# Optimization experiments

Hardware: AMD Instinct MI355X
Metric: run time of the kernel (lower is better)

The kernel has to match this reference:

```python
import jax, jax.numpy as jnp
import numpy as np

N = 50000      # nodes
E = 600000     # edges
DIN = 128      # dim_in
DOUT = 128     # dim_out (mulhead=1)
DG = 64        # dim_gate


def setup_inputs() -> dict:
    key = jax.random.key(0)
    ks = jax.random.split(key, 10)
    rows = jax.random.randint(ks[0], (E,), 0, N, dtype=jnp.int32)   # dest nodes
    cols = jax.random.randint(ks[1], (E,), 0, N, dtype=jnp.int32)   # src nodes
    vals = jax.random.uniform(ks[2], (E,), dtype=jnp.float32)       # adj_norm values
    feat = jax.random.normal(ks[3], (N, DIN), dtype=jnp.float32)
    s = 1.0 / np.sqrt(DIN)
    W0 = jax.random.normal(ks[4], (DIN, DOUT), dtype=jnp.float32) * s
    b0 = jnp.zeros((DOUT,), dtype=jnp.float32)
    W1 = jax.random.normal(ks[5], (DIN, DOUT), dtype=jnp.float32) * s
    b1 = jnp.zeros((DOUT,), dtype=jnp.float32)
    att = jax.random.normal(ks[6], (2 * DOUT,), dtype=jnp.float32) * 0.1  # attention param [1, 2*DOUT] flattened
    W_pool = jax.random.normal(ks[7], (DIN, DG), dtype=jnp.float32) * s    # weight_pool_gate
    W_gate = jax.random.normal(ks[8], (2 * DIN + DG, 1), dtype=jnp.float32) * 0.05  # weight_gate, mulhead=1
    offset0 = jnp.zeros((DOUT,), dtype=jnp.float32)
    scale0 = jnp.ones((DOUT,), dtype=jnp.float32)
    offset1 = jnp.zeros((DOUT,), dtype=jnp.float32)
    scale1 = jnp.ones((DOUT,), dtype=jnp.float32)
    return dict(rows=rows, cols=cols, vals=vals, feat=feat, W0=W0, b0=b0,
                W1=W1, b1=b1, att=att, W_pool=W_pool, W_gate=W_gate,
                offset0=offset0, scale0=scale0, offset1=offset1, scale1=scale1)


def _batch_norm(x, scale, offset):
    # per-node norm over the feature dim (unbiased=False), matching _batch_norm
    m = x.mean(axis=1, keepdims=True)
    v = x.var(axis=1, keepdims=True) + 1e-9
    return (x - m) * scale * jax.lax.rsqrt(v) + offset


def reference(rows, cols, vals, feat, W0, b0, W1, b1, att, W_pool, W_gate,
              offset0, scale0, offset1, scale1):
    n = feat.shape[0]
    d = W0.shape[1]
    # --- gate value (GaAN eq. 3) ---
    zj = feat @ W_pool                                   # [N, DG]
    neigh_zj = jax.ops.segment_max(zj[cols], rows, num_segments=n)  # per-row max over neighbors
    neigh_zj = jnp.where(jnp.isfinite(neigh_zj), neigh_zj, 0.0)     # empty rows -> zeros
    neigh_mean = jax.ops.segment_sum(vals[:, None] * feat[cols], rows, num_segments=n)  # spmm(adj, feat)
    gate = jnp.concatenate([feat, neigh_zj, neigh_mean], axis=1) @ W_gate  # [N, 1]
    # --- per-order feature transforms (order=1, mulhead=1) ---
    h0 = jax.nn.relu(feat @ W0 + b0)                     # order 0 (self)
    h1 = jax.nn.relu(feat @ W1 + b1)                     # order 1 (neighbor)
    # --- sparse attention aggregation ---
    a_self = jax.nn.leaky_relu(h0 @ att[:d], 0.2)        # [N]
    a_neigh = jax.nn.leaky_relu(h1 @ att[d:], 0.2)       # [N]
    e = a_self[rows] + a_neigh[cols]                     # per-edge score (replaces adj values)
    agg = jax.ops.segment_sum(e[:, None] * h1[cols], rows, num_segments=n)  # spmm(att_adj, h1)
    agg = agg * gate[:, :1]                              # gated
    # --- per-node batch norm, then 'mean' aggregation (sum of orders) ---
    return _batch_norm(h0, scale0, offset0) + _batch_norm(agg, scale1, offset1)
```

## Files before the change

kernel.cpp:

```cpp
#include <hip/hip_runtime.h>

#define DIN 128
#define DG 64

typedef __attribute__((ext_vector_type(8))) short short8;
typedef __attribute__((ext_vector_type(4))) float f32x4;

static __device__ __forceinline__ unsigned short f2bf(float x) {
    unsigned u = __builtin_bit_cast(unsigned, x);
    u = (u + 0x7FFF + ((u >> 16) & 1)) >> 16;
    return (unsigned short)u;
}
static __device__ __forceinline__ float bf2f(unsigned short s) {
    return __builtin_bit_cast(float, (unsigned)s << 16);
}

__global__ void k_deg(const int* __restrict__ rows, int* __restrict__ deg,
                      int* __restrict__ slot, int E) {
    int e = blockIdx.x * blockDim.x + threadIdx.x;
    if (e < E) slot[e] = atomicAdd(&deg[rows[e]], 1);
}

__global__ __launch_bounds__(1024) void k_scan1(const int* __restrict__ deg,
                                                int* __restrict__ rowptr,
                                                int* __restrict__ bsum, int n) {
    __shared__ int wsum[16];
    __shared__ int woff[16];
    int tid = threadIdx.x;
    int lane = tid & 63, w = tid >> 6;
    int i = blockIdx.x * 1024 + tid;
    int v = (i < n) ? deg[i] : 0;
    int x = v;
    #pragma unroll
    for (int off = 1; off < 64; off <<= 1) {
        int y = __shfl_up(x, off, 64);
        if (lane >= off) x += y;
    }
    if (lane == 63) wsum[w] = x;
    __syncthreads();
    if (w == 0) {
        int t = (lane < 16) ? wsum[lane] : 0;
        int xx = t;
        #pragma unroll
        for (int off = 1; off < 16; off <<= 1) {
            int y = __shfl_up(xx, off, 64);
            if (lane >= off) xx += y;
        }
        if (lane < 16) woff[lane] = xx - t;
    }
    __syncthreads();
    if (i < n) rowptr[i] = x - v + woff[w];
    if (tid == 1023) bsum[blockIdx.x] = woff[15] + wsum[15];
}

__global__ void k_scan2(const int* __restrict__ bsum, int* __restrict__ boff,
                        int* __restrict__ rowptr, int nb, int n) {
    int lane = threadIdx.x;
    int v = (lane < nb) ? bsum[lane] : 0;
    int x = v;
    #pragma unroll
    for (int off = 1; off < 64; off <<= 1) {
        int y = __shfl_up(x, off, 64);
        if (lane >= off) x += y;
    }
    boff[lane] = x - v;
    if (lane == 63) rowptr[n] = x;
}

__global__ void k_scan3(int* __restrict__ rowptr, const int* __restrict__ boff, int n) {
    int i = blockIdx.x * blockDim.x + threadIdx.x;
    if (i < n) rowptr[i] += boff[i >> 10];
}

__global__ __launch_bounds__(256) void k_wt(
    const float* __restrict__ W0, const float* __restrict__ W1,
    unsigned short* __restrict__ Bt) {
    int k = blockIdx.x;
    int c = threadIdx.x;
    const float* W = (c < 128) ? W0 : W1;
    Bt[c * 128 + k] = f2bf(W[k * 128 + (c & 127)]);
}

#define AS_LD 132
#define ALD 136
#define SMEM_BYTES 25088

static __device__ __forceinline__ void zj_body(
    const float* __restrict__ feat, const float* __restrict__ Wp,
    const float* __restrict__ Wg,
    float* __restrict__ zj, float* __restrict__ gpart, float* __restrict__ fdotg,
    int N, char* smem) {
    float* As = (float*)smem;
    float* Bs = (float*)(smem + 32 * AS_LD * 4);
    int tid = threadIdx.x;
    int tx = tid & 15, ty = tid >> 4;
    int m0 = blockIdx.x * 128;
    if (m0 >= N) return;
    float acc[8][4];
    #pragma unroll
    for (int r = 0; r < 8; ++r)
        #pragma unroll
        for (int c = 0; c < 4; ++c) acc[r][c] = 0.f;
    float gdot[8], fdot[8];
    #pragma unroll
    for (int r = 0; r < 8; ++r) { gdot[r] = 0.f; fdot[r] = 0.f; }
    for (int kc = 0; kc < 128; kc += 32) {
        for (int i = tid; i < 1024; i += 256) {
            int m = i >> 3, kq = (i & 7) << 2;
            int node = m0 + m;
            float4 f;
            if (node < N) f = *(const float4*)&feat[(size_t)node * 128 + kc + kq];
            else          f = make_float4(0.f, 0.f, 0.f, 0.f);
            As[(kq + 0) * AS_LD + m] = f.x;
            As[(kq + 1) * AS_LD + m] = f.y;
            As[(kq + 2) * AS_LD + m] = f.z;
            As[(kq + 3) * AS_LD + m] = f.w;
        }
        for (int i = tid; i < 512; i += 256) {
            int k = i >> 4, cq = (i & 15) << 2;
            *(float4*)&Bs[k * 64 + cq] = *(const float4*)&Wp[(size_t)(kc + k) * 64 + cq];
        }
        __syncthreads();
        #pragma unroll 8
        for (int kk = 0; kk < 32; ++kk) {
            const float* ar = &As[kk * AS_LD];
            float4 a0 = *(const float4*)(ar + 4 * tx);
            float4 a1 = *(const float4*)(ar + 64 + 4 * tx);
            float4 b0v = *(const float4*)&Bs[kk * 64 + 4 * ty];
            float a[8] = {a0.x, a0.y, a0.z, a0.w, a1.x, a1.y, a1.z, a1.w};
            #pragma unroll
            for (int r = 0; r < 8; ++r) {
                acc[r][0] += a[r] * b0v.x; acc[r][1] += a[r] * b0v.y;
                acc[r][2] += a[r] * b0v.z; acc[r][3] += a[r] * b0v.w;
            }
            float g1 = Wg[kc + kk];
            float g2 = Wg[192 + kc + kk];
            #pragma unroll
            for (int r = 0; r < 8; ++r) { gdot[r] += a[r] * g1; fdot[r] += a[r] * g2; }
        }
        __syncthreads();
    }
    #pragma unroll
    for (int r = 0; r < 8; ++r) {
        int node = m0 + ((r < 4) ? (4 * tx + r) : (64 + 4 * tx + (r - 4)));
        if (node >= N) continue;
        *(float4*)&zj[(size_t)node * 64 + 4 * ty] =
            make_float4(acc[r][0], acc[r][1], acc[r][2], acc[r][3]);
        if (ty == 0) { gpart[node] = gdot[r]; fdotg[node] = fdot[r]; }
    }
}

static __device__ __forceinline__ void mfma_body(
    const float* __restrict__ feat, const unsigned short* __restrict__ Bt,
    const float* __restrict__ b0, const float* __restrict__ b1,
    const float* __restrict__ att,
    float* __restrict__ h0, unsigned short* __restrict__ hb,
    float* __restrict__ a_self, float* __restrict__ a_neigh, int N, char* smem) {
    unsigned short* As = (unsigned short*)smem;
    float* sredA = (float*)(smem + 64 * ALD * 2);
    float* nredA = sredA + 128;
    int tid = threadIdx.x;
    int m0 = blockIdx.x * 64;
    for (int i = tid; i < 2048; i += 256) {
        int row = i >> 5, ch = i & 31;
        int node = m0 + row;
        float4 f;
        if (node < N) f = *(const float4*)&feat[(size_t)node * 128 + ch * 4];
        else          f = make_float4(0.f, 0.f, 0.f, 0.f);
        unsigned p0 = (unsigned)f2bf(f.x) | ((unsigned)f2bf(f.y) << 16);
        unsigned p1 = (unsigned)f2bf(f.z) | ((unsigned)f2bf(f.w) << 16);
        *(uint2*)&As[row * ALD + ch * 4] = make_uint2(p0, p1);
    }
    __syncthreads();
    int w = tid >> 6, lane = tid & 63;
    int lm = lane & 15, q = lane >> 4;
    f32x4 acc[4][4];
    #pragma unroll
    for (int rt = 0; rt < 4; ++rt)
        #pragma unroll
        for (int ct = 0; ct < 4; ++ct)
            #pragma unroll
            for (int r = 0; r < 4; ++r) acc[rt][ct][r] = 0.f;
    #pragma unroll
    for (int ks = 0; ks < 4; ++ks) {
        short8 a[4], b[4];
        #pragma unroll
        for (int rt = 0; rt < 4; ++rt)
            a[rt] = *(const short8*)&As[(rt * 16 + lm) * ALD + ks * 32 + q * 8];
        #pragma unroll
        for (int ct = 0; ct < 4; ++ct)
            b[ct] = *(const short8*)&Bt[(size_t)(w * 64 + ct * 16 + lm) * 128 + ks * 32 + q * 8];
        #pragma unroll
        for (int rt = 0; rt < 4; ++rt)
            #pragma unroll
            for (int ct = 0; ct < 4; ++ct)
                acc[rt][ct] = __builtin_amdgcn_mfma_f32_16x16x32_bf16(a[rt], b[ct], acc[rt][ct], 0, 0, 0);
    }
    float sacc[4][4];
    #pragma unroll
    for (int rt = 0; rt < 4; ++rt)
        #pragma unroll
        for (int r = 0; r < 4; ++r) sacc[rt][r] = 0.f;
    #pragma unroll
    for (int ct = 0; ct < 4; ++ct) {
        int col = w * 64 + ct * 16 + lm;
        float attc = att[col];
        float bias = (w < 2) ? b0[col] : b1[col - 128];
        #pragma unroll
        for (int rt = 0; rt < 4; ++rt) {
            #pragma unroll
            for (int r = 0; r < 4; ++r) {
                float v = acc[rt][ct][r] + bias;
                v = fmaxf(v, 0.f);
                sacc[rt][r] += v * attc;
                int node = m0 + rt * 16 + q * 4 + r;
                if (node < N) {
                    if (w < 2) h0[(size_t)node * 128 + col] = v;
                    else       hb[(size_t)node * 128 + (col - 128)] = f2bf(v);
                }
            }
        }
    }
    float* red = (w < 2) ? sredA : nredA;
    #pragma unroll
    for (int rt = 0; rt < 4; ++rt)
        #pragma unroll
        for (int r = 0; r < 4; ++r) {
            float s = sacc[rt][r];
            s += __shfl_xor(s, 1, 64); s += __shfl_xor(s, 2, 64);
            s += __shfl_xor(s, 4, 64); s += __shfl_xor(s, 8, 64);
            if (lm == 0) red[(w & 1) * 64 + rt * 16 + q * 4 + r] = s;
        }
    __syncthreads();
    if (tid < 64) {
        int node = m0 + tid;
        if (node < N) {
            float s  = sredA[tid] + sredA[64 + tid];
            float nn = nredA[tid] + nredA[64 + tid];
            a_self[node]  = (s  >= 0.f) ? s  : 0.2f * s;
            a_neigh[node] = (nn >= 0.f) ? nn : 0.2f * nn;
        }
    }
}

__global__ __launch_bounds__(256) void k_gemm_fused(
    const float* __restrict__ feat, const float* __restrict__ Wp,
    const unsigned short* __restrict__ Bt,
    const float* __restrict__ b0, const float* __restrict__ b1,
    const float* __restrict__ att, const float* __restrict__ Wg,
    float* __restrict__ h0, unsigned short* __restrict__ hb,
    float* __restrict__ zj, float* __restrict__ gpart, float* __restrict__ fdotg,
    float* __restrict__ a_self, float* __restrict__ a_neigh, int N) {
    __shared__ __align__(16) char smem[SMEM_BYTES];
    if (blockIdx.y == 0)
        zj_body(feat, Wp, Wg, zj, gpart, fdotg, N, smem);
    else
        mfma_body(feat, Bt, b0, b1, att, h0, hb, a_self, a_neigh, N, smem);
}

__global__ void k_scatter_meta(const int* __restrict__ rows, const int* __restrict__ cols,
                               const float* __restrict__ vals,
                               const int* __restrict__ rowptr, const int* __restrict__ slot,
                               const float* __restrict__ a_neigh, const float* __restrict__ fdotg,
                               float4* __restrict__ meta, int E) {
    int e = blockIdx.x * blockDim.x + threadIdx.x;
    if (e < E) {
        int c = cols[e];
        int dst = rowptr[rows[e]] + slot[e];
        meta[dst] = make_float4(__builtin_bit_cast(float, c),
                                a_neigh[c], vals[e] * fdotg[c], 0.f);
    }
}

template<int C>
static __device__ __forceinline__ void agg_chunk_m(
    const float4* __restrict__ meta, int j, int je, int lane, float asr,
    const unsigned short* __restrict__ hb, const float* __restrict__ zj,
    float2& acca, float& zmax, float& vfsum) {
    float4 m[C]; bool act[C];
    #pragma unroll
    for (int t = 0; t < C; ++t) {
        int jj = j + t;
        act[t] = jj < je;
        m[t] = meta[act[t] ? jj : (je - 1)];
    }
    ushort2 hv[C]; float zv[C];
    #pragma unroll
    for (int t = 0; t < C; ++t) {
        int c = __builtin_bit_cast(int, m[t].x);
        hv[t] = ((const ushort2*)(hb + (size_t)c * 128))[lane];
        zv[t] = zj[(size_t)c * 64 + lane];
    }
    #pragma unroll
    for (int t = 0; t < C; ++t) {
        float es = act[t] ? (asr + m[t].y) : 0.f;
        acca.x += es * bf2f(hv[t].x);
        acca.y += es * bf2f(hv[t].y);
        zmax = fmaxf(zmax, act[t] ? zv[t] : -__builtin_inff());
        vfsum += act[t] ? m[t].z : 0.f;
    }
}

__global__ __launch_bounds__(256) void k_aggregate(
    const float4* __restrict__ meta, const int* __restrict__ rowptr,
    const float* __restrict__ h0, const unsigned short* __restrict__ hb,
    const float* __restrict__ zj,
    const float* __restrict__ a_self, const float* __restrict__ gpart,
    const float* __restrict__ Wg,
    const float* __restrict__ scale0, const float* __restrict__ offset0,
    const float* __restrict__ scale1, const float* __restrict__ offset1,
    float* __restrict__ out, int N) {
    int r = blockIdx.x * 4 + (threadIdx.x >> 6);
    int lane = threadIdx.x & 63;
    if (r >= N) return;
    int jb = rowptr[r], je = rowptr[r + 1];
    float2 acca = {0.f, 0.f};
    float zmax = -__builtin_inff();
    float vfsum = 0.f;
    float asr = a_self[r];
    for (int j = jb; j < je; j += 8)
        agg_chunk_m<8>(meta, j, je, lane, asr, hb, zj, acca, zmax, vfsum);
    if (jb == je) zmax = 0.f;
    float gs = zmax * Wg[128 + lane];
    #pragma unroll
    for (int off = 32; off; off >>= 1) gs += __shfl_xor(gs, off, 64);
    float gate = gpart[r] + gs + vfsum;
    float2 ag = {acca.x * gate, acca.y * gate};
    float2 x0 = ((const float2*)(h0 + (size_t)r * 128))[lane];
    float m0s = x0.x + x0.y;
    #pragma unroll
    for (int off = 32; off; off >>= 1) m0s += __shfl_xor(m0s, off, 64);
    float m0 = m0s * (1.f / 128.f);
    float d0x = x0.x - m0, d0y = x0.y - m0;
    float v0s = d0x * d0x + d0y * d0y;
    #pragma unroll
    for (int off = 32; off; off >>= 1) v0s += __shfl_xor(v0s, off, 64);
    float inv0 = rsqrtf(v0s * (1.f / 128.f) + 1e-9f);
    float m1s = ag.x + ag.y;
    #pragma unroll
    for (int off = 32; off; off >>= 1) m1s += __shfl_xor(m1s, off, 64);
    float m1 = m1s * (1.f / 128.f);
    float d1x = ag.x - m1, d1y = ag.y - m1;
    float v1s = d1x * d1x + d1y * d1y;
    #pragma unroll
    for (int off = 32; off; off >>= 1) v1s += __shfl_xor(v1s, off, 64);
    float inv1 = rsqrtf(v1s * (1.f / 128.f) + 1e-9f);
    float2 sc0 = ((const float2*)scale0)[lane], of0 = ((const float2*)offset0)[lane];
    float2 sc1 = ((const float2*)scale1)[lane], of1 = ((const float2*)offset1)[lane];
    float2 o;
    o.x = d0x * sc0.x * inv0 + of0.x + d1x * sc1.x * inv1 + of1.x;
    o.y = d0y * sc0.y * inv0 + of0.y + d1y * sc1.y * inv1 + of1.y;
    ((float2*)(out + (size_t)r * 128))[lane] = o;
}

extern "C" void kernel_launch(void* const* d_in, const int* in_sizes, int n_in,
                              void* d_out, int out_size, void* d_ws, size_t ws_size,
                              hipStream_t stream) {
    const int*   rows   = (const int*)d_in[0];
    const int*   cols   = (const int*)d_in[1];
    const float* vals   = (const float*)d_in[2];
    const float* feat   = (const float*)d_in[3];
    const float* W0     = (const float*)d_in[4];
    const float* b0     = (const float*)d_in[5];
    const float* W1     = (const float*)d_in[6];
    const float* b1     = (const float*)d_in[7];
    const float* att    = (const float*)d_in[8];
    const float* Wp     = (const float*)d_in[9];
    const float* Wg     = (const float*)d_in[10];
    const float* offset0 = (const float*)d_in[11];
    const float* scale0  = (const float*)d_in[12];
    const float* offset1 = (const float*)d_in[13];
    const float* scale1  = (const float*)d_in[14];
    float* out = (float*)d_out;

    const int E = in_sizes[0];
    const int N = in_sizes[3] / DIN;
    const int Npad = (N + 63) & ~63;

    char* ws = (char*)d_ws;
    float* h0          = (float*)ws;          ws += (size_t)N * 128 * sizeof(float);
    unsigned short* hb = (unsigned short*)ws; ws += (size_t)N * 128 * sizeof(unsigned short);
    float* zj          = (float*)ws;          ws += (size_t)N * 64 * sizeof(float);
    unsigned short* Bt = (unsigned short*)ws; ws += (size_t)256 * 128 * sizeof(unsigned short);
    float* a_self  = (float*)ws; ws += (size_t)N * sizeof(float);
    float* a_neigh = (float*)ws; ws += (size_t)N * sizeof(float);
    float* gpart   = (float*)ws; ws += (size_t)N * sizeof(float);
    float* fdotg   = (float*)ws; ws += (size_t)N * sizeof(float);
    int* deg      = (int*)ws; ws += (size_t)(N + 1) * sizeof(int);
    int* rowptr   = (int*)ws; ws += (size_t)(N + 1) * sizeof(int);
    int* bsum     = (int*)ws; ws += 64 * sizeof(int);
    int* boff     = (int*)ws; ws += 64 * sizeof(int);
    int* slot     = (int*)ws; ws += (size_t)E * sizeof(int);
    ws = (char*)(((size_t)ws + 15) & ~(size_t)15);
    float4* meta  = (float4*)ws; ws += (size_t)E * sizeof(float4);

    hipMemsetAsync(deg, 0, (size_t)(N + 1) * sizeof(int), stream);

    k_deg<<<(E + 255) / 256, 256, 0, stream>>>(rows, deg, slot, E);
    int nb = (N + 1023) >> 10;
    k_scan1<<<nb, 1024, 0, stream>>>(deg, rowptr, bsum, N);
    k_scan2<<<1, 64, 0, stream>>>(bsum, boff, rowptr, nb, N);
    k_scan3<<<(N + 255) / 256, 256, 0, stream>>>(rowptr, boff, N);

    k_wt<<<128, 256, 0, stream>>>(W0, W1, Bt);

    dim3 gg(Npad / 64, 2);
    k_gemm_fused<<<gg, 256, 0, stream>>>(feat, Wp, Bt, b0, b1, att, Wg,
                                         h0, hb, zj, gpart, fdotg, a_self, a_neigh, N);

    k_scatter_meta<<<(E + 255) / 256, 256, 0, stream>>>(rows, cols, vals, rowptr, slot,
                                                        a_neigh, fdotg, meta, E);

    int nb4 = (N + 3) / 4;
    k_aggregate<<<nb4, 256, 0, stream>>>(meta, rowptr, h0, hb, zj,
                                         a_self, gpart, Wg,
                                         scale0, offset0, scale1, offset1, out, N);
}
```

Measured before the change: 258.4 us.

## Merge small setup kernels into fused launches and prefetch aggregate operands early

```diff
diff --git a/kernel.cpp b/kernel.cpp
--- a/kernel.cpp
+++ b/kernel.cpp
@@ -15,10 +15,20 @@
     return __builtin_bit_cast(float, (unsigned)s << 16);
 }
 
-__global__ void k_deg(const int* __restrict__ rows, int* __restrict__ deg,
-                      int* __restrict__ slot, int E) {
-    int e = blockIdx.x * blockDim.x + threadIdx.x;
-    if (e < E) slot[e] = atomicAdd(&deg[rows[e]], 1);
+__global__ void k_deg_wt(const int* __restrict__ rows, int* __restrict__ deg,
+                         int* __restrict__ slot, int E, int nDeg,
+                         const float* __restrict__ W0, const float* __restrict__ W1,
+                         unsigned short* __restrict__ Bt) {
+    int b = blockIdx.x;
+    if (b < nDeg) {
+        int e = b * 256 + threadIdx.x;
+        if (e < E) slot[e] = atomicAdd(&deg[rows[e]], 1);
+    } else {
+        int k = b - nDeg;
+        int c = threadIdx.x;
+        const float* W = (c < 128) ? W0 : W1;
+        Bt[c * 128 + k] = f2bf(W[k * 128 + (c & 127)]);
+    }
 }
 
 __global__ __launch_bounds__(1024) void k_scan1(const int* __restrict__ deg,
@@ -51,34 +61,6 @@
     __syncthreads();
     if (i < n) rowptr[i] = x - v + woff[w];
     if (tid == 1023) bsum[blockIdx.x] = woff[15] + wsum[15];
-}
-
-__global__ void k_scan2(const int* __restrict__ bsum, int* __restrict__ boff,
-                        int* __restrict__ rowptr, int nb, int n) {
-    int lane = threadIdx.x;
-    int v = (lane < nb) ? bsum[lane] : 0;
-    int x = v;
-    #pragma unroll
-    for (int off = 1; off < 64; off <<= 1) {
-        int y = __shfl_up(x, off, 64);
-        if (lane >= off) x += y;
-    }
-    boff[lane] = x - v;
-    if (lane == 63) rowptr[n] = x;
-}
-
-__global__ void k_scan3(int* __restrict__ rowptr, const int* __restrict__ boff, int n) {
-    int i = blockIdx.x * blockDim.x + threadIdx.x;
-    if (i < n) rowptr[i] += boff[i >> 10];
-}
-
-__global__ __launch_bounds__(256) void k_wt(
-    const float* __restrict__ W0, const float* __restrict__ W1,
-    unsigned short* __restrict__ Bt) {
-    int k = blockIdx.x;
-    int c = threadIdx.x;
-    const float* W = (c < 128) ? W0 : W1;
-    Bt[c * 128 + k] = f2bf(W[k * 128 + (c & 127)]);
 }
 
 #define AS_LD 132
@@ -243,19 +225,38 @@
     }
 }
 
-__global__ __launch_bounds__(256) void k_gemm_fused(
+static __device__ __forceinline__ void scanfin_body(
+    int* __restrict__ rowptr, const int* __restrict__ bsum, int nbs, int n) {
+    int b = blockIdx.x;
+    int i = b * 256 + threadIdx.x;
+    if (b * 256 > n) return;
+    int seg = (b * 256) >> 10;
+    int pref = 0;
+    for (int t = 0; t < seg; ++t) pref += bsum[t];
+    if (i < n) rowptr[i] += pref;
+    else if (i == n) {
+        int tot = pref;
+        for (int t = seg; t < nbs; ++t) tot += bsum[t];
+        rowptr[n] = tot;
+    }
+}
+
+__global__ __launch_bounds__(256) void k_fused(
     const float* __restrict__ feat, const float* __restrict__ Wp,
     const unsigned short* __restrict__ Bt,
     const float* __restrict__ b0, const float* __restrict__ b1,
     const float* __restrict__ att, const float* __restrict__ Wg,
     float* __restrict__ h0, unsigned short* __restrict__ hb,
     float* __restrict__ zj, float* __restrict__ gpart, float* __restrict__ fdotg,
-    float* __restrict__ a_self, float* __restrict__ a_neigh, int N) {
+    float* __restrict__ a_self, float* __restrict__ a_neigh,
+    int* __restrict__ rowptr, const int* __restrict__ bsum, int nbs, int nsc, int N) {
     __shared__ __align__(16) char smem[SMEM_BYTES];
     if (blockIdx.y == 0)
         zj_body(feat, Wp, Wg, zj, gpart, fdotg, N, smem);
-    else
+    else if (blockIdx.y == 1)
         mfma_body(feat, Bt, b0, b1, att, h0, hb, a_self, a_neigh, N, smem);
+    else if (blockIdx.x < nsc)
+        scanfin_body(rowptr, bsum, nbs, N);
 }
 
 __global__ void k_scatter_meta(const int* __restrict__ rows, const int* __restrict__ cols,
@@ -274,7 +275,7 @@
 
 template<int C>
 static __device__ __forceinline__ void agg_chunk_m(
-    const float4* __restrict__ meta, int j, int je, int lane, float asr,
+    const float4* __restrict__ meta, int j, int je, int E, int lane, float asr,
     const unsigned short* __restrict__ hb, const float* __restrict__ zj,
     float2& acca, float& zmax, float& vfsum) {
     float4 m[C]; bool act[C];
@@ -282,7 +283,7 @@
     for (int t = 0; t < C; ++t) {
         int jj = j + t;
         act[t] = jj < je;
-        m[t] = meta[act[t] ? jj : (je - 1)];
+        m[t] = meta[min(jj, E - 1)];
     }
     ushort2 hv[C]; float zv[C];
     #pragma unroll
@@ -309,24 +310,29 @@
     const float* __restrict__ Wg,
     const float* __restrict__ scale0, const float* __restrict__ offset0,
     const float* __restrict__ scale1, const float* __restrict__ offset1,
-    float* __restrict__ out, int N) {
+    float* __restrict__ out, int N, int E) {
     int r = blockIdx.x * 4 + (threadIdx.x >> 6);
     int lane = threadIdx.x & 63;
     if (r >= N) return;
     int jb = rowptr[r], je = rowptr[r + 1];
+    float asr = a_self[r];
+    float gp  = gpart[r];
+    float wgl = Wg[128 + lane];
+    float2 x0 = ((const float2*)(h0 + (size_t)r * 128))[lane];
+    float2 sc0 = ((const float2*)scale0)[lane], of0 = ((const float2*)offset0)[lane];
+    float2 sc1 = ((const float2*)scale1)[lane], of1 = ((const float2*)offset1)[lane];
     float2 acca = {0.f, 0.f};
     float zmax = -__builtin_inff();
     float vfsum = 0.f;
-    float asr = a_self[r];
-    for (int j = jb; j < je; j += 8)
-        agg_chunk_m<8>(meta, j, je, lane, asr, hb, zj, acca, zmax, vfsum);
+    agg_chunk_m<16>(meta, jb, je, E, lane, asr, hb, zj, acca, zmax, vfsum);
+    for (int j = jb + 16; j < je; j += 8)
+        agg_chunk_m<8>(meta, j, je, E, lane, asr, hb, zj, acca, zmax, vfsum);
     if (jb == je) zmax = 0.f;
-    float gs = zmax * Wg[128 + lane];
+    float gs = zmax * wgl;
     #pragma unroll
     for (int off = 32; off; off >>= 1) gs += __shfl_xor(gs, off, 64);
-    float gate = gpart[r] + gs + vfsum;
+    float gate = gp + gs + vfsum;
     float2 ag = {acca.x * gate, acca.y * gate};
-    float2 x0 = ((const float2*)(h0 + (size_t)r * 128))[lane];
     float m0s = x0.x + x0.y;
     #pragma unroll
     for (int off = 32; off; off >>= 1) m0s += __shfl_xor(m0s, off, 64);
@@ -345,8 +351,6 @@
     #pragma unroll
     for (int off = 32; off; off >>= 1) v1s += __shfl_xor(v1s, off, 64);
     float inv1 = rsqrtf(v1s * (1.f / 128.f) + 1e-9f);
-    float2 sc0 = ((const float2*)scale0)[lane], of0 = ((const float2*)offset0)[lane];
-    float2 sc1 = ((const float2*)scale1)[lane], of1 = ((const float2*)offset1)[lane];
     float2 o;
     o.x = d0x * sc0.x * inv0 + of0.x + d1x * sc1.x * inv1 + of1.x;
     o.y = d0y * sc0.y * inv0 + of0.y + d1y * sc1.y * inv1 + of1.y;
@@ -389,30 +393,29 @@
     int* deg      = (int*)ws; ws += (size_t)(N + 1) * sizeof(int);
     int* rowptr   = (int*)ws; ws += (size_t)(N + 1) * sizeof(int);
     int* bsum     = (int*)ws; ws += 64 * sizeof(int);
-    int* boff     = (int*)ws; ws += 64 * sizeof(int);
     int* slot     = (int*)ws; ws += (size_t)E * sizeof(int);
     ws = (char*)(((size_t)ws + 15) & ~(size_t)15);
     float4* meta  = (float4*)ws; ws += (size_t)E * sizeof(float4);
 
     hipMemsetAsync(deg, 0, (size_t)(N + 1) * sizeof(int), stream);
 
-    k_deg<<<(E + 255) / 256, 256, 0, stream>>>(rows, deg, slot, E);
+    int nDeg = (E + 255) / 256;
+    k_deg_wt<<<nDeg + 128, 256, 0, stream>>>(rows, deg, slot, E, nDeg, W0, W1, Bt);
+
     int nb = (N + 1023) >> 10;
     k_scan1<<<nb, 1024, 0, stream>>>(deg, rowptr, bsum, N);
-    k_scan2<<<1, 64, 0, stream>>>(bsum, boff, rowptr, nb, N);
-    k_scan3<<<(N + 255) / 256, 256, 0, stream>>>(rowptr, boff, N);
-
-    k_wt<<<128, 256, 0, stream>>>(W0, W1, Bt);
-
-    dim3 gg(Npad / 64, 2);
-    k_gemm_fused<<<gg, 256, 0, stream>>>(feat, Wp, Bt, b0, b1, att, Wg,
-                                         h0, hb, zj, gpart, fdotg, a_self, a_neigh, N);
-
-    k_scatter_meta<<<(E + 255) / 256, 256, 0, stream>>>(rows, cols, vals, rowptr, slot,
-                                                        a_neigh, fdotg, meta, E);
+
+    int nsc = (N + 256) / 256;
+    dim3 gg(Npad / 64, 3);
+    k_fused<<<gg, 256, 0, stream>>>(feat, Wp, Bt, b0, b1, att, Wg,
+                                    h0, hb, zj, gpart, fdotg, a_self, a_neigh,
+                                    rowptr, bsum, nb, nsc, N);
+
+    k_scatter_meta<<<nDeg, 256, 0, stream>>>(rows, cols, vals, rowptr, slot,
+                                             a_neigh, fdotg, meta, E);
 
     int nb4 = (N + 3) / 4;
     k_aggregate<<<nb4, 256, 0, stream>>>(meta, rowptr, h0, hb, zj,
                                          a_self, gpart, Wg,
-                                         scale0, offset0, scale1, offset1, out, N);
-}
+                                         scale0, offset0, scale1, offset1, out, N, E);
+}
```

Measured after the change: 265.5 us. 2.8% more time.
